# Performance work log

Measured on AMD Instinct MI355X. Metric: run time of the kernel, lower is better.

## Reference

```python
import jax, jax.numpy as jnp
import numpy as np

B, T, D_MODEL, HEAD_DIM = 4, 4096, 2048, 128
NEG = -1e9  # matches torch's -1000000000.0 mask fill


def setup_inputs() -> dict:
    key = jax.random.key(0)
    ks = jax.random.split(key, 7)
    s = 0.02
    return {
        "x": jax.random.normal(ks[0], (B, T, D_MODEL), dtype=jnp.float32),
        "q_w": jax.random.normal(ks[1], (HEAD_DIM, D_MODEL), dtype=jnp.float32) * s,
        "q_b": jax.random.normal(ks[2], (HEAD_DIM,), dtype=jnp.float32) * s,
        "k_w": jax.random.normal(ks[3], (HEAD_DIM, D_MODEL), dtype=jnp.float32) * s,
        "k_b": jax.random.normal(ks[4], (HEAD_DIM,), dtype=jnp.float32) * s,
        "v_w": jax.random.normal(ks[5], (HEAD_DIM, D_MODEL), dtype=jnp.float32) * s,
        "v_b": jax.random.normal(ks[6], (HEAD_DIM,), dtype=jnp.float32) * s,
    }


def reference(x, q_w, q_b, k_w, k_b, v_w, v_b):
    # Linear projections: y = x @ W^T + b  -> [B, T, head_dim]
    q = jnp.einsum("btc,hc->bth", x, q_w) + q_b
    k = jnp.einsum("btc,hc->bth", x, k_w) + k_b
    v = jnp.einsum("btc,hc->bth", x, v_w) + v_b

    head_dim = q.shape[-1]
    # scores [B, T, T], scaled by 1/sqrt(head_dim)
    scores = jnp.einsum("bqh,bkh->bqk", q, k) / jnp.sqrt(jnp.float32(head_dim))
    # causal mask: additive -1e9 above the diagonal (future positions)
    t = scores.shape[-1]
    mask = jnp.triu(jnp.full((t, t), NEG, dtype=scores.dtype), k=1)
    scores = scores + mask
    probs = jax.nn.softmax(scores, axis=-1)
    # dropout p=0.0 -> identity (eval)
    y = jnp.einsum("bqk,bkh->bqh", probs, v)
    return y
```

## Files before the change

kernel.cpp:

```cpp
#include <hip/hip_runtime.h>

#define T_SEQ 4096
#define DMODEL 2048
#define HD 128

typedef float f32x4 __attribute__((ext_vector_type(4)));
typedef _Float16 f16x8 __attribute__((ext_vector_type(8)));

__device__ __forceinline__ unsigned short f2h(float f) {
  union { _Float16 h; unsigned short u; } v;
  v.h = (_Float16)f;
  return v.u;
}

__device__ __forceinline__ unsigned pk2h(float lo, float hi) {
  return (unsigned)f2h(lo) | ((unsigned)f2h(hi) << 16);
}

template <int CTRL>
__device__ __forceinline__ float dppmax(float x) {
  union { float f; int i; } a, b;
  a.f = x;
  b.i = __builtin_amdgcn_update_dpp(a.i, a.i, CTRL, 0xF, 0xF, false);
  return fmaxf(x, b.f);
}
template <int CTRL>
__device__ __forceinline__ float dppadd(float x) {
  union { float f; int i; } a, b;
  a.f = x;
  b.i = __builtin_amdgcn_update_dpp(a.i, a.i, CTRL, 0xF, 0xF, false);
  return x + b.f;
}
__device__ __forceinline__ float red16_max(float x) {
  x = dppmax<0xB1>(x); x = dppmax<0x4E>(x);
  x = dppmax<0x124>(x); x = dppmax<0x128>(x);
  return x;
}
__device__ __forceinline__ float red16_add(float x) {
  x = dppadd<0xB1>(x); x = dppadd<0x4E>(x);
  x = dppadd<0x124>(x); x = dppadd<0x128>(x);
  return x;
}

__global__ __launch_bounds__(256) void cvt_w_kernel(
    const float* __restrict__ qw, const float* __restrict__ qb,
    const float* __restrict__ kw, const float* __restrict__ kb,
    const float* __restrict__ vw, const float* __restrict__ vb,
    unsigned short* __restrict__ wb, float* __restrict__ biasc) {
  int idx = blockIdx.x * 256 + threadIdx.x;
  int e = idx * 4;
  int row = e >> 11;
  int col = e & 2047;
  const float* src = (row < 128) ? (qw + row * 2048)
                   : (row < 256) ? (kw + (row - 128) * 2048)
                                 : (vw + (row - 256) * 2048);
  float4 v = *(const float4*)(src + col);
  ushort4 o;
  o.x = f2h(v.x); o.y = f2h(v.y); o.z = f2h(v.z); o.w = f2h(v.w);
  *(ushort4*)(wb + e) = o;
  if (blockIdx.x == 0 && threadIdx.x < 384) {
    int n = threadIdx.x;
    biasc[n] = (n < 128) ? qb[n] : (n < 256) ? kb[n - 128] : vb[n - 256];
  }
}

#define SAB 40
__global__ __launch_bounds__(256, 3) void proj_kernel(
    const float* __restrict__ x, const unsigned short* __restrict__ wb,
    const float* __restrict__ biasc, unsigned short* __restrict__ qkv) {
  __shared__ unsigned short sA[64 * SAB];
  __shared__ unsigned short sB[128 * SAB];
  const int tid = threadIdx.x;
  const int lane = tid & 63;
  const int w = tid >> 6;
  const int fr = lane & 15;
  const int g = lane >> 4;
  const int m0 = blockIdx.x * 64;
  const int n0 = blockIdx.y * 128;
  const int wm = (w & 1) * 32;
  const int wn = (w >> 1) * 64;

  const int arow = tid >> 2;
  const int acolA = (tid & 3) * 8;
  const int brow = tid >> 1;
  const int bcolB = (tid & 1) * 16;
  const float* xp = x + (size_t)(m0 + arow) * DMODEL + acolA;
  const unsigned short* bp = wb + (size_t)(n0 + brow) * DMODEL + bcolB;

  f32x4 acc[2][4] = {};
  float4 ax0 = *(const float4*)(xp);
  float4 ax1 = *(const float4*)(xp + 4);
  uint4 bx0 = *(const uint4*)(bp);
  uint4 bx1 = *(const uint4*)(bp + 8);

  for (int k0 = 0; k0 < DMODEL; k0 += 32) {
    __syncthreads();
    uint4 pa;
    pa.x = pk2h(ax0.x, ax0.y); pa.y = pk2h(ax0.z, ax0.w);
    pa.z = pk2h(ax1.x, ax1.y); pa.w = pk2h(ax1.z, ax1.w);
    *(uint4*)&sA[arow * SAB + acolA] = pa;
    *(uint4*)&sB[brow * SAB + bcolB] = bx0;
    *(uint4*)&sB[brow * SAB + bcolB + 8] = bx1;
    __syncthreads();

    if (k0 + 32 < DMODEL) {
      ax0 = *(const float4*)(xp + k0 + 32);
      ax1 = *(const float4*)(xp + k0 + 36);
      bx0 = *(const uint4*)(bp + k0 + 32);
      bx1 = *(const uint4*)(bp + k0 + 40);
    }

    f16x8 af[2], bf[4];
#pragma unroll
    for (int i = 0; i < 2; ++i)
      af[i] = *(const f16x8*)&sA[(wm + 16 * i + fr) * SAB + g * 8];
#pragma unroll
    for (int jn = 0; jn < 4; ++jn)
      bf[jn] = *(const f16x8*)&sB[(wn + 16 * jn + fr) * SAB + g * 8];
#pragma unroll
    for (int i = 0; i < 2; ++i)
#pragma unroll
      for (int jn = 0; jn < 4; ++jn)
        acc[i][jn] = __builtin_amdgcn_mfma_f32_16x16x32_f16(af[i], bf[jn], acc[i][jn], 0, 0, 0);
  }

#pragma unroll
  for (int jn = 0; jn < 4; ++jn) {
    int n = n0 + wn + 16 * jn + fr;
    float bias = biasc[n];
#pragma unroll
    for (int i = 0; i < 2; ++i) {
      int mb = m0 + wm + 16 * i + g * 4;
#pragma unroll
      for (int r = 0; r < 4; ++r)
        qkv[(size_t)(mb + r) * 384 + n] = f2h(acc[i][jn][r] + bias);
    }
  }
}

#define SKS 136
#define SVS 72
#define SPS 72
__global__ __launch_bounds__(256) __attribute__((amdgpu_waves_per_eu(2, 3)))
void attn_kernel(
    const unsigned short* __restrict__ qkv, float* __restrict__ out,
    float* __restrict__ po, float* __restrict__ pml, int split) {
  __shared__ unsigned short sK[64 * SKS];
  __shared__ unsigned short sVt[128 * SVS];
  __shared__ unsigned short sP[64 * SPS];
  const int id = blockIdx.x;
  const int batch = blockIdx.y;
  int qt, c, nc;
  if (split) {
    if (id < 16)      { qt = id;                c = 0;          nc = 1; }
    else if (id < 48) { qt = 16 + ((id - 16) >> 1); c = (id - 16) & 1; nc = 2; }
    else if (id < 96) { qt = 32 + (id - 48) / 3;    c = (id - 48) % 3; nc = 3; }
    else              { qt = 48 + ((id - 96) >> 2); c = (id - 96) & 3; nc = 4; }
  } else { qt = id; c = 0; nc = 1; }
  const int qbase = qt * 64;
  const int ntl = qt + 1;
  const int t0 = (c * ntl) / nc;
  const int tend = ((c + 1) * ntl) / nc;
  const int tid = threadIdx.x;
  const int lane = tid & 63;
  const int w = tid >> 6;
  const int fr = lane & 15;
  const int g = lane >> 4;
  const int va = tid >> 4;
  const int vu = tid & 15;
  const int vblk = ((va ^ (vu & 14)) << 2);
  const unsigned short* qkvb = qkv + (size_t)batch * T_SEQ * 384;

  f16x8 qf[4];
  {
    const unsigned short* qp = qkvb + (size_t)(qbase + 16 * w + fr) * 384 + g * 8;
#pragma unroll
    for (int s = 0; s < 4; ++s) qf[s] = *(const f16x8*)(qp + 32 * s);
  }
  f32x4 o[8] = {};
  float m_r[4], l_r[4];
#pragma unroll
  for (int r = 0; r < 4; ++r) { m_r[r] = -1e30f; l_r[r] = 0.f; }
  const float scale = 0.08838834764831845f;

  uint4 pk[4], pvv[4];
#pragma unroll
  for (int it = 0; it < 4; ++it) {
    int idx = it * 256 + tid;
    pk[it] = *(const uint4*)(qkvb + (size_t)(t0 * 64 + (idx >> 4)) * 384 + 128 + (idx & 15) * 8);
  }
#pragma unroll
  for (int i = 0; i < 4; ++i)
    pvv[i] = *(const uint4*)(qkvb + (size_t)(t0 * 64 + va + 16 * i) * 384 + 256 + vu * 8);

  for (int t = t0; t < tend; ++t) {
    const int kbase = t * 64;
    __syncthreads();
#pragma unroll
    for (int it = 0; it < 4; ++it) {
      int idx = it * 256 + tid;
      *(uint4*)&sK[(idx >> 4) * SKS + (idx & 15) * 8] = pk[it];
    }
    {
      const unsigned* w0 = (const unsigned*)&pvv[0];
      const unsigned* w1 = (const unsigned*)&pvv[1];
      const unsigned* w2 = (const unsigned*)&pvv[2];
      const unsigned* w3 = (const unsigned*)&pvv[3];
#pragma unroll
      for (int j2 = 0; j2 < 4; ++j2) {
        uint2 se, so;
        se.x = __builtin_amdgcn_perm(w1[j2], w0[j2], 0x05040100);
        se.y = __builtin_amdgcn_perm(w3[j2], w2[j2], 0x05040100);
        so.x = __builtin_amdgcn_perm(w1[j2], w0[j2], 0x07060302);
        so.y = __builtin_amdgcn_perm(w3[j2], w2[j2], 0x07060302);
        *(uint2*)&sVt[(8 * vu + 2 * j2) * SVS + vblk] = se;
        *(uint2*)&sVt[(8 * vu + 2 * j2 + 1) * SVS + vblk] = so;
      }
    }
    __syncthreads();

    if (t + 1 < tend) {
#pragma unroll
      for (int it = 0; it < 4; ++it) {
        int idx = it * 256 + tid;
        pk[it] = *(const uint4*)(qkvb + (size_t)((t + 1) * 64 + (idx >> 4)) * 384 + 128 + (idx & 15) * 8);
      }
#pragma unroll
      for (int i = 0; i < 4; ++i)
        pvv[i] = *(const uint4*)(qkvb + (size_t)((t + 1) * 64 + va + 16 * i) * 384 + 256 + vu * 8);
    }

    f32x4 sacc[4] = {};
#pragma unroll
    for (int ks = 0; ks < 4; ++ks)
#pragma unroll
      for (int tn = 0; tn < 4; ++tn) {
        f16x8 kf = *(const f16x8*)&sK[(16 * tn + fr) * SKS + 32 * ks + g * 8];
        sacc[tn] = __builtin_amdgcn_mfma_f32_16x16x32_f16(qf[ks], kf, sacc[tn], 0, 0, 0);
      }

    const bool diag = (t == qt);
    float pv[4][4];
#pragma unroll
    for (int r = 0; r < 4; ++r) {
      int grow = qbase + 16 * w + g * 4 + r;
      float mx = -1e30f;
#pragma unroll
      for (int tn = 0; tn < 4; ++tn) {
        float s = sacc[tn][r] * scale;
        if (diag && (kbase + 16 * tn + fr) > grow) s = -1e30f;
        pv[tn][r] = s;
        mx = fmaxf(mx, s);
      }
      mx = red16_max(mx);
      float mnew = fmaxf(m_r[r], mx);
      float alpha = __expf(m_r[r] - mnew);
      m_r[r] = mnew;
      float rs = 0.f;
#pragma unroll
      for (int tn = 0; tn < 4; ++tn) {
        float p = __expf(pv[tn][r] - mnew);
        pv[tn][r] = p;
        rs += p;
      }
      rs = red16_add(rs);
      l_r[r] = l_r[r] * alpha + rs;
#pragma unroll
      for (int nt = 0; nt < 8; ++nt) o[nt][r] *= alpha;
    }

#pragma unroll
    for (int r = 0; r < 4; ++r) {
      uint2 pw;
      pw.x = pk2h(pv[0][r], pv[1][r]);
      pw.y = pk2h(pv[2][r], pv[3][r]);
      *(uint2*)&sP[(16 * w + 4 * g + r) * SPS + 4 * fr] = pw;
    }

#pragma unroll
    for (int ks = 0; ks < 2; ++ks) {
      f16x8 pa = *(const f16x8*)&sP[(16 * w + fr) * SPS + 32 * ks + 8 * g];
#pragma unroll
      for (int nt = 0; nt < 8; ++nt) {
        int d = 16 * nt + fr;
        int blk = ((8 * ks + 2 * g) ^ ((d >> 3) & 14)) << 2;
        f16x8 vf = *(const f16x8*)&sVt[d * SVS + blk];
        o[nt] = __builtin_amdgcn_mfma_f32_16x16x32_f16(pa, vf, o[nt], 0, 0, 0);
      }
    }
  }

  if (nc == 1) {
#pragma unroll
    for (int r = 0; r < 4; ++r) {
      float inv = 1.0f / l_r[r];
      int grow = qbase + 16 * w + g * 4 + r;
      float* op = out + ((size_t)batch * T_SEQ + grow) * HD;
#pragma unroll
      for (int nt = 0; nt < 8; ++nt)
        op[16 * nt + fr] = o[nt][r] * inv;
    }
  } else {
    size_t slot = ((size_t)batch * 160 + id) * 64;
#pragma unroll
    for (int r = 0; r < 4; ++r) {
      int lrow = 16 * w + g * 4 + r;
      float* op = po + (slot + lrow) * 128;
#pragma unroll
      for (int nt = 0; nt < 8; ++nt)
        op[16 * nt + fr] = o[nt][r];
      if (fr == 0) {
        pml[(slot + lrow) * 2] = m_r[r];
        pml[(slot + lrow) * 2 + 1] = l_r[r];
      }
    }
  }
}

__global__ __launch_bounds__(256) void combine_kernel(
    const float* __restrict__ po, const float* __restrict__ pml,
    float* __restrict__ out) {
  int gr = blockIdx.x * 2 + (threadIdx.x >> 7);
  int d = threadIdx.x & 127;
  int batch = gr / 3072;
  int ridx = gr - batch * 3072;
  int qt = 16 + (ridx >> 6);
  int rr = ridx & 63;
  int nc = 1 + (qt >> 4);
  int sb = (qt < 32) ? 16 + (qt - 16) * 2
         : (qt < 48) ? 48 + (qt - 32) * 3
                     : 96 + (qt - 48) * 4;
  size_t base = ((size_t)batch * 160 + sb) * 64 + rr;
  float mi[4], li[4];
  float M = -1e30f;
#pragma unroll
  for (int i = 0; i < 4; ++i) {
    if (i < nc) {
      mi[i] = pml[(base + (size_t)i * 64) * 2];
      li[i] = pml[(base + (size_t)i * 64) * 2 + 1];
      M = fmaxf(M, mi[i]);
    }
  }
  float L = 0.f, acc = 0.f;
#pragma unroll
  for (int i = 0; i < 4; ++i) {
    if (i < nc) {
      float sc = __expf(mi[i] - M);
      L += li[i] * sc;
      acc += po[(base + (size_t)i * 64) * 128 + d] * sc;
    }
  }
  out[((size_t)batch * T_SEQ + qt * 64 + rr) * HD + d] = acc / L;
}

extern "C" void kernel_launch(void* const* d_in, const int* in_sizes, int n_in,
                              void* d_out, int out_size, void* d_ws, size_t ws_size,
                              hipStream_t stream) {
  const float* x  = (const float*)d_in[0];
  const float* qw = (const float*)d_in[1];
  const float* qb = (const float*)d_in[2];
  const float* kw = (const float*)d_in[3];
  const float* kb = (const float*)d_in[4];
  const float* vw = (const float*)d_in[5];
  const float* vb = (const float*)d_in[6];
  float* out = (float*)d_out;

  unsigned short* qkv = (unsigned short*)d_ws;
  unsigned short* wb  = qkv + (size_t)16384 * 384;
  float* biasc = (float*)(wb + (size_t)384 * 2048);
  float* po  = (float*)((char*)d_ws + 14157312);
  float* pml = po + (size_t)640 * 64 * 128;
  size_t need = 14157312 + (size_t)640 * 64 * 128 * 4 + (size_t)640 * 64 * 2 * 4;
  int split = (ws_size >= need) ? 1 : 0;

  cvt_w_kernel<<<768, 256, 0, stream>>>(qw, qb, kw, kb, vw, vb, wb, biasc);
  proj_kernel<<<dim3(256, 3), 256, 0, stream>>>(x, wb, biasc, qkv);
  attn_kernel<<<dim3(split ? 160 : 64, 4), 256, 0, stream>>>(qkv, out, po, pml, split);
  if (split)
    combine_kernel<<<6144, 256, 0, stream>>>(po, pml, out);
}
```

Before: 141.6 us.

## Use lazy softmax rescaling, defer next-tile prefetch, and drop waves_per_eu hint

The online-softmax update now rescales the output accumulators and row sum only when the new row max exceeds the running max by more than 8, skipping the per-tile multiply of 32 accumulators in the common case. The next tile's K/V global prefetch is moved to after the QK^T MMA and softmax so its registers are not live during that section, and the causal-mask check is simplified. The waves_per_eu attribute is removed, which gives the compiler freedom over register allocation and occupancy. The lazy threshold lets exponentials reach up to e^8 before rescaling, which the fp16 P values must tolerate, and later loads give less latency hiding.

```diff
diff --git a/kernel.cpp b/kernel.cpp
--- a/kernel.cpp
+++ b/kernel.cpp
@@ -141,8 +141,7 @@
 #define SKS 136
 #define SVS 72
 #define SPS 72
-__global__ __launch_bounds__(256) __attribute__((amdgpu_waves_per_eu(2, 3)))
-void attn_kernel(
+__global__ __launch_bounds__(256) void attn_kernel(
     const unsigned short* __restrict__ qkv, float* __restrict__ out,
     float* __restrict__ po, float* __restrict__ pml, int split) {
   __shared__ unsigned short sK[64 * SKS];
@@ -219,6 +218,52 @@
     }
     __syncthreads();
 
+    f32x4 sacc[4] = {};
+#pragma unroll
+    for (int ks = 0; ks < 4; ++ks)
+#pragma unroll
+      for (int tn = 0; tn < 4; ++tn) {
+        f16x8 kf = *(const f16x8*)&sK[(16 * tn + fr) * SKS + 32 * ks + g * 8];
+        sacc[tn] = __builtin_amdgcn_mfma_f32_16x16x32_f16(qf[ks], kf, sacc[tn], 0, 0, 0);
+      }
+
+    const bool diag = (t == qt);
+#pragma unroll
+    for (int r = 0; r < 4; ++r) {
+      int grow = qbase + 16 * w + g * 4 + r;
+      float s0 = sacc[0][r] * scale;
+      float s1 = sacc[1][r] * scale;
+      float s2 = sacc[2][r] * scale;
+      float s3 = sacc[3][r] * scale;
+      if (diag) {
+        int kd = grow - kbase - fr;
+        if (0 > kd)  s0 = -1e30f;
+        if (16 > kd) s1 = -1e30f;
+        if (32 > kd) s2 = -1e30f;
+        if (48 > kd) s3 = -1e30f;
+      }
+      float mx = fmaxf(fmaxf(s0, s1), fmaxf(s2, s3));
+      mx = red16_max(mx);
+      if (mx > m_r[r] + 8.0f) {
+        float alpha = __expf(m_r[r] - mx);
+        m_r[r] = mx;
+        l_r[r] *= alpha;
+#pragma unroll
+        for (int nt = 0; nt < 8; ++nt) o[nt][r] *= alpha;
+      }
+      float p0 = __expf(s0 - m_r[r]);
+      float p1 = __expf(s1 - m_r[r]);
+      float p2 = __expf(s2 - m_r[r]);
+      float p3 = __expf(s3 - m_r[r]);
+      float rs = (p0 + p1) + (p2 + p3);
+      rs = red16_add(rs);
+      l_r[r] += rs;
+      uint2 pw;
+      pw.x = pk2h(p0, p1);
+      pw.y = pk2h(p2, p3);
+      *(uint2*)&sP[(16 * w + 4 * g + r) * SPS + 4 * fr] = pw;
+    }
+
     if (t + 1 < tend) {
 #pragma unroll
       for (int it = 0; it < 4; ++it) {
@@ -228,53 +273,6 @@
 #pragma unroll
       for (int i = 0; i < 4; ++i)
         pvv[i] = *(const uint4*)(qkvb + (size_t)((t + 1) * 64 + va + 16 * i) * 384 + 256 + vu * 8);
-    }
-
-    f32x4 sacc[4] = {};
-#pragma unroll
-    for (int ks = 0; ks < 4; ++ks)
-#pragma unroll
-      for (int tn = 0; tn < 4; ++tn) {
-        f16x8 kf = *(const f16x8*)&sK[(16 * tn + fr) * SKS + 32 * ks + g * 8];
-        sacc[tn] = __builtin_amdgcn_mfma_f32_16x16x32_f16(qf[ks], kf, sacc[tn], 0, 0, 0);
-      }
-
-    const bool diag = (t == qt);
-    float pv[4][4];
-#pragma unroll
-    for (int r = 0; r < 4; ++r) {
-      int grow = qbase + 16 * w + g * 4 + r;
-      float mx = -1e30f;
-#pragma unroll
-      for (int tn = 0; tn < 4; ++tn) {
-        float s = sacc[tn][r] * scale;
-        if (diag && (kbase + 16 * tn + fr) > grow) s = -1e30f;
-        pv[tn][r] = s;
-        mx = fmaxf(mx, s);
-      }
-      mx = red16_max(mx);
-      float mnew = fmaxf(m_r[r], mx);
-      float alpha = __expf(m_r[r] - mnew);
-      m_r[r] = mnew;
-      float rs = 0.f;
-#pragma unroll
-      for (int tn = 0; tn < 4; ++tn) {
-        float p = __expf(pv[tn][r] - mnew);
-        pv[tn][r] = p;
-        rs += p;
-      }
-      rs = red16_add(rs);
-      l_r[r] = l_r[r] * alpha + rs;
-#pragma unroll
-      for (int nt = 0; nt < 8; ++nt) o[nt][r] *= alpha;
-    }
-
-#pragma unroll
-    for (int r = 0; r < 4; ++r) {
-      uint2 pw;
-      pw.x = pk2h(pv[0][r], pv[1][r]);
-      pw.y = pk2h(pv[2][r], pv[3][r]);
-      *(uint2*)&sP[(16 * w + 4 * g + r) * SPS + 4 * fr] = pw;
     }
 
 #pragma unroll
```

Result: slower. 153.2 us (+8.2%).

## Double projection K-tile to 64 and switch softmax to base-2 exponent

Applied to the files above, without the earlier changes.

The projection GEMM now stages a 64-wide K slice per iteration instead of 32, using wider shared tiles, twice the register prefetch, and two MFMA sub-steps per barrier pair, and it drops the occupancy hint from launch bounds. This halves the number of syncthreads round-trips and loop overhead at the cost of more registers and LDS. In attention, the score scale is folded together with log2(e) so the softmax and combine steps can use exp2f instead of __expf, which saves a multiply per exponential. The base-2 max and sum values stay consistent through the merge kernel.

```diff
diff --git a/kernel.cpp b/kernel.cpp
--- a/kernel.cpp
+++ b/kernel.cpp
@@ -64,8 +64,8 @@
   }
 }
 
-#define SAB 40
-__global__ __launch_bounds__(256, 3) void proj_kernel(
+#define SAB 72
+__global__ __launch_bounds__(256) void proj_kernel(
     const float* __restrict__ x, const unsigned short* __restrict__ wb,
     const float* __restrict__ biasc, unsigned short* __restrict__ qkv) {
   __shared__ unsigned short sA[64 * SAB];
@@ -81,47 +81,63 @@
   const int wn = (w >> 1) * 64;
 
   const int arow = tid >> 2;
-  const int acolA = (tid & 3) * 8;
+  const int acol = (tid & 3) * 16;
   const int brow = tid >> 1;
-  const int bcolB = (tid & 1) * 16;
-  const float* xp = x + (size_t)(m0 + arow) * DMODEL + acolA;
-  const unsigned short* bp = wb + (size_t)(n0 + brow) * DMODEL + bcolB;
+  const int bcol = (tid & 1) * 32;
+  const float* xp = x + (size_t)(m0 + arow) * DMODEL + acol;
+  const unsigned short* bp = wb + (size_t)(n0 + brow) * DMODEL + bcol;
 
   f32x4 acc[2][4] = {};
   float4 ax0 = *(const float4*)(xp);
   float4 ax1 = *(const float4*)(xp + 4);
+  float4 ax2 = *(const float4*)(xp + 8);
+  float4 ax3 = *(const float4*)(xp + 12);
   uint4 bx0 = *(const uint4*)(bp);
   uint4 bx1 = *(const uint4*)(bp + 8);
-
-  for (int k0 = 0; k0 < DMODEL; k0 += 32) {
+  uint4 bx2 = *(const uint4*)(bp + 16);
+  uint4 bx3 = *(const uint4*)(bp + 24);
+
+  for (int k0 = 0; k0 < DMODEL; k0 += 64) {
     __syncthreads();
-    uint4 pa;
-    pa.x = pk2h(ax0.x, ax0.y); pa.y = pk2h(ax0.z, ax0.w);
-    pa.z = pk2h(ax1.x, ax1.y); pa.w = pk2h(ax1.z, ax1.w);
-    *(uint4*)&sA[arow * SAB + acolA] = pa;
-    *(uint4*)&sB[brow * SAB + bcolB] = bx0;
-    *(uint4*)&sB[brow * SAB + bcolB + 8] = bx1;
+    uint4 pa0, pa1;
+    pa0.x = pk2h(ax0.x, ax0.y); pa0.y = pk2h(ax0.z, ax0.w);
+    pa0.z = pk2h(ax1.x, ax1.y); pa0.w = pk2h(ax1.z, ax1.w);
+    pa1.x = pk2h(ax2.x, ax2.y); pa1.y = pk2h(ax2.z, ax2.w);
+    pa1.z = pk2h(ax3.x, ax3.y); pa1.w = pk2h(ax3.z, ax3.w);
+    *(uint4*)&sA[arow * SAB + acol]     = pa0;
+    *(uint4*)&sA[arow * SAB + acol + 8] = pa1;
+    *(uint4*)&sB[brow * SAB + bcol]      = bx0;
+    *(uint4*)&sB[brow * SAB + bcol + 8]  = bx1;
+    *(uint4*)&sB[brow * SAB + bcol + 16] = bx2;
+    *(uint4*)&sB[brow * SAB + bcol + 24] = bx3;
     __syncthreads();
 
-    if (k0 + 32 < DMODEL) {
-      ax0 = *(const float4*)(xp + k0 + 32);
-      ax1 = *(const float4*)(xp + k0 + 36);
-      bx0 = *(const uint4*)(bp + k0 + 32);
-      bx1 = *(const uint4*)(bp + k0 + 40);
-    }
-
-    f16x8 af[2], bf[4];
-#pragma unroll
-    for (int i = 0; i < 2; ++i)
-      af[i] = *(const f16x8*)&sA[(wm + 16 * i + fr) * SAB + g * 8];
-#pragma unroll
-    for (int jn = 0; jn < 4; ++jn)
-      bf[jn] = *(const f16x8*)&sB[(wn + 16 * jn + fr) * SAB + g * 8];
-#pragma unroll
-    for (int i = 0; i < 2; ++i)
+    if (k0 + 64 < DMODEL) {
+      ax0 = *(const float4*)(xp + k0 + 64);
+      ax1 = *(const float4*)(xp + k0 + 68);
+      ax2 = *(const float4*)(xp + k0 + 72);
+      ax3 = *(const float4*)(xp + k0 + 76);
+      bx0 = *(const uint4*)(bp + k0 + 64);
+      bx1 = *(const uint4*)(bp + k0 + 72);
+      bx2 = *(const uint4*)(bp + k0 + 80);
+      bx3 = *(const uint4*)(bp + k0 + 88);
+    }
+
+#pragma unroll
+    for (int ks = 0; ks < 2; ++ks) {
+      f16x8 af[2], bf[4];
+#pragma unroll
+      for (int i = 0; i < 2; ++i)
+        af[i] = *(const f16x8*)&sA[(wm + 16 * i + fr) * SAB + ks * 32 + g * 8];
 #pragma unroll
       for (int jn = 0; jn < 4; ++jn)
-        acc[i][jn] = __builtin_amdgcn_mfma_f32_16x16x32_f16(af[i], bf[jn], acc[i][jn], 0, 0, 0);
+        bf[jn] = *(const f16x8*)&sB[(wn + 16 * jn + fr) * SAB + ks * 32 + g * 8];
+#pragma unroll
+      for (int i = 0; i < 2; ++i)
+#pragma unroll
+        for (int jn = 0; jn < 4; ++jn)
+          acc[i][jn] = __builtin_amdgcn_mfma_f32_16x16x32_f16(af[i], bf[jn], acc[i][jn], 0, 0, 0);
+    }
   }
 
 #pragma unroll
@@ -181,7 +197,7 @@
   float m_r[4], l_r[4];
 #pragma unroll
   for (int r = 0; r < 4; ++r) { m_r[r] = -1e30f; l_r[r] = 0.f; }
-  const float scale = 0.08838834764831845f;
+  const float c2 = 0.12751742f;
 
   uint4 pk[4], pvv[4];
 #pragma unroll
@@ -247,19 +263,19 @@
       float mx = -1e30f;
 #pragma unroll
       for (int tn = 0; tn < 4; ++tn) {
-        float s = sacc[tn][r] * scale;
+        float s = sacc[tn][r] * c2;
         if (diag && (kbase + 16 * tn + fr) > grow) s = -1e30f;
         pv[tn][r] = s;
         mx = fmaxf(mx, s);
       }
       mx = red16_max(mx);
       float mnew = fmaxf(m_r[r], mx);
-      float alpha = __expf(m_r[r] - mnew);
+      float alpha = exp2f(m_r[r] - mnew);
       m_r[r] = mnew;
       float rs = 0.f;
 #pragma unroll
       for (int tn = 0; tn < 4; ++tn) {
-        float p = __expf(pv[tn][r] - mnew);
+        float p = exp2f(pv[tn][r] - mnew);
         pv[tn][r] = p;
         rs += p;
       }
@@ -345,7 +361,7 @@
 #pragma unroll
   for (int i = 0; i < 4; ++i) {
     if (i < nc) {
-      float sc = __expf(mi[i] - M);
+      float sc = exp2f(mi[i] - M);
       L += li[i] * sc;
       acc += po[(base + (size_t)i * 64) * 128 + d] * sc;
     }
```

Measured after the change: 154.9 us. 1.09x slower.
